# Performance work log

Measured on AMD Instinct MI355X. Metric: run time of the kernel, lower is better.

## Reference

```python
import jax, jax.numpy as jnp
import numpy as np

B, N, E = 256, 512, 8192
F_IN, DEPTH, NHID = 128, 3, 256
CAT = F_IN + DEPTH * NHID  # 896


def setup_inputs() -> dict:
    key = jax.random.key(0)
    ks = jax.random.split(key, 20)
    def w(k, shape, fan_in):
        return jax.random.normal(k, shape, jnp.float32) / np.sqrt(fan_in)
    inp = {
        "x": jax.random.normal(ks[0], (B, N, F_IN), jnp.float32),
        "edge_index": jax.random.randint(ks[1], (2, E), 0, N, jnp.int64),
        # linears: first maps F_IN->NHID, rest NHID->NHID (stacked)
        "lin0_W": w(ks[2], (F_IN, NHID), F_IN),
        "lin0_b": jnp.zeros((NHID,), jnp.float32),
        "lin_Ws": w(ks[3], (DEPTH - 1, NHID, NHID), NHID),
        "lin_bs": jnp.zeros((DEPTH - 1, NHID), jnp.float32),
        # GCNConv weights (stacked), PyG semantics: A_norm (X W) + b
        "conv_Ws": w(ks[4], (DEPTH, NHID, NHID), NHID),
        "conv_bs": jnp.zeros((DEPTH, NHID), jnp.float32),
        "sig_W": w(ks[5], (CAT, NHID), CAT),
        "sig_b": jnp.zeros((NHID,), jnp.float32),
        "tanh_W": w(ks[6], (CAT, NHID), CAT),
        "tanh_b": jnp.zeros((NHID,), jnp.float32),
        "f1_W": w(ks[7], (NHID, NHID), NHID),
        "f1_b": jnp.zeros((NHID,), jnp.float32),
        "f2_W": w(ks[8], (NHID, 2), NHID),
        "f2_b": jnp.zeros((2,), jnp.float32),
    }
    return inp


def _gcn_norm(edge_index, n):
    # add self loops, compute symmetric normalization D^-1/2 (A+I) D^-1/2
    loop = jnp.arange(n, dtype=edge_index.dtype)
    src = jnp.concatenate([edge_index[0], loop])
    dst = jnp.concatenate([edge_index[1], loop])
    deg = jax.ops.segment_sum(jnp.ones_like(src, jnp.float32), dst, num_segments=n)
    dinv = jax.lax.rsqrt(jnp.maximum(deg, 1.0))
    norm = dinv[src] * dinv[dst]  # [E+N]
    return src, dst, norm


def _gcn(h, W, b, src, dst, norm, n):
    # h: [B, N, C]
    hW = h @ W
    msg = hW[:, src, :] * norm[None, :, None]          # [B, E+N, C]
    agg = jax.vmap(lambda m: jax.ops.segment_sum(m, dst, num_segments=n))(msg)
    return agg + b


def reference(x, edge_index, lin0_W, lin0_b, lin_Ws, lin_bs, conv_Ws, conv_bs,
              sig_W, sig_b, tanh_W, tanh_b, f1_W, f1_b, f2_W, f2_b):
    n = x.shape[1]
    src, dst, norm = _gcn_norm(edge_index, n)
    xs = [x]
    out = x
    for i in range(DEPTH):
        if i == 0:
            out = out @ lin0_W + lin0_b
        else:
            out = out @ lin_Ws[i - 1] + lin_bs[i - 1]
        out = _gcn(out, conv_Ws[i], conv_bs[i], src, dst, norm, n)
        out = jnp.tanh(out)
        xs.append(out)
    cat = jnp.concatenate(xs, axis=-1)                 # [B, N, CAT]
    s = jax.nn.sigmoid(cat @ sig_W + sig_b)            # [B, N, NHID]
    t = jnp.tanh(cat @ tanh_W + tanh_b)                # [B, N, NHID]
    pooled = jnp.sum(s * t, axis=1)                    # [B, NHID] (sum over nodes)
    embeds = jnp.tanh(pooled)
    h = jax.nn.relu(embeds @ f1_W + f1_b)              # dropout is eval-mode identity
    preds = h @ f2_W + f2_b                            # [B, 2]
    preds = jnp.concatenate([jax.nn.sigmoid(preds[:, :1]), preds[:, 1:]], axis=-1)
    return preds, embeds
```

## Files before the change

### kernel.cpp

```cpp
#include <hip/hip_runtime.h>
#include <hip/hip_bf16.h>
#include <cstdint>

typedef _Float16 half_t;
typedef __attribute__((ext_vector_type(8))) _Float16 half8;
typedef __attribute__((ext_vector_type(4))) _Float16 half4;
typedef __attribute__((ext_vector_type(4))) float f32x4;

#define MFMA16x32(a, b, c) __builtin_amdgcn_mfma_f32_16x16x32_f16(a, b, c, 0, 0, 0)

static constexpr int NB  = 256;
static constexpr int NN  = 512;
static constexpr int NE  = 8192;
static constexpr int FIN = 128;
static constexpr int NH  = 256;
static constexpr int CAT = 896;

__device__ __forceinline__ void gload16(const half_t* __restrict__ g, half_t* l)
{
    __builtin_amdgcn_global_load_lds(
        (const __attribute__((address_space(1))) uint32_t*)(uintptr_t)g,
        (__attribute__((address_space(3))) uint32_t*)(uintptr_t)l, 16, 0, 0);
}

__device__ __forceinline__ void stage128x64(
    const half_t* __restrict__ src, long row0, int ldk, int k0,
    half_t* lds, int tid)
{
    const int wid = tid >> 6, lane = tid & 63;
#pragma unroll
    for (int it = 0; it < 4; ++it) {
        const int rb   = wid * 32 + it * 8;
        const int row  = rb + (lane >> 3);
        const int slot = (lane & 7) ^ (row & 7);
        gload16(src + (row0 + row) * (long)ldk + k0 + slot * 8,
                lds + (size_t)rb * 64);
    }
}

__device__ __forceinline__ half8 fragr(const half_t* lds, int row, int slot)
{
    return *(const half8*)(lds + row * 64 + ((slot ^ (row & 7)) * 8));
}

struct Tab {
    const void* src[16];
    float*      dst[16];
    int         n[16];
    int         fi[16];
    int         nseg;
};

__global__ void k_detect_all(Tab t, int* __restrict__ flags)
{
    const int s = blockIdx.x;
    if (s >= t.nseg) return;
    __shared__ int cnt_s;
    if (threadIdx.x == 0) cnt_s = 0;
    __syncthreads();
    const uint32_t* w = (const uint32_t*)t.src[s];
    int nw = t.n[s] / 2; if (nw > 2048) nw = 2048; if (nw < 1) nw = 1;
    int c = 0;
    for (int i = threadIdx.x; i < nw; i += 256) {
        const uint32_t lo = w[i] & 0xFFFFu;
        const int e = (int)((lo >> 7) & 0xFF);
        if (lo == 0u || (e >= 116 && e <= 136)) ++c;
    }
    atomicAdd(&cnt_s, c);
    __syncthreads();
    if (threadIdx.x == 0) flags[t.fi[s]] = (2 * cnt_s >= nw) ? 1 : 0;
}

__global__ void k_cvt_all(Tab t, const int* __restrict__ flags)
{
    for (int s = 0; s < t.nseg; ++s) {
        float* dst = t.dst[s];
        if (dst == nullptr) continue;
        const int is_bf = flags[t.fi[s]];
        const int n = t.n[s];
        const void* src = t.src[s];
        for (int i = blockIdx.x * 256 + threadIdx.x; i < n; i += gridDim.x * 256)
            dst[i] = is_bf
                ? __uint_as_float(((uint32_t)((const uint16_t*)src)[i]) << 16)
                : ((const float*)src)[i];
    }
}

__global__ void k_x2h(const void* __restrict__ xraw, size_t elem_off,
                      half_t* __restrict__ o, size_t n8, const int* __restrict__ flag)
{
    const int is_bf = *flag;
    const size_t gid0 = (size_t)blockIdx.x * blockDim.x + threadIdx.x;
    const size_t stride = (size_t)gridDim.x * blockDim.x;
    if (is_bf) {
        const uint4* src = (const uint4*)((const uint16_t*)xraw + elem_off);
        for (size_t i = gid0; i < n8; i += stride) {
            const uint4 v = src[i];
            half8 h;
            h[0] = (_Float16)__uint_as_float((v.x & 0xFFFFu) << 16);
            h[1] = (_Float16)__uint_as_float(v.x & 0xFFFF0000u);
            h[2] = (_Float16)__uint_as_float((v.y & 0xFFFFu) << 16);
            h[3] = (_Float16)__uint_as_float(v.y & 0xFFFF0000u);
            h[4] = (_Float16)__uint_as_float((v.z & 0xFFFFu) << 16);
            h[5] = (_Float16)__uint_as_float(v.z & 0xFFFF0000u);
            h[6] = (_Float16)__uint_as_float((v.w & 0xFFFFu) << 16);
            h[7] = (_Float16)__uint_as_float(v.w & 0xFFFF0000u);
            ((half8*)o)[i] = h;
        }
    } else {
        const float4* src = (const float4*)((const float*)xraw + elem_off);
        for (size_t i = gid0; i < n8; i += stride) {
            const float4 a = src[2 * i], b = src[2 * i + 1];
            half8 h;
            h[0] = (_Float16)a.x; h[1] = (_Float16)a.y;
            h[2] = (_Float16)a.z; h[3] = (_Float16)a.w;
            h[4] = (_Float16)b.x; h[5] = (_Float16)b.y;
            h[6] = (_Float16)b.z; h[7] = (_Float16)b.w;
            ((half8*)o)[i] = h;
        }
    }
}

__global__ void k_world(const int* __restrict__ fl, int* __restrict__ w4)
{
    if (threadIdx.x == 0) {
        const int any = fl[0] | fl[1] | fl[2] | fl[3] | fl[4] | fl[5] | fl[6];
        *w4 = any ? 0 : 1;
    }
}

__global__ void k_sentinel(__hip_bfloat16* __restrict__ out, float code)
{
    const int i = blockIdx.x * 256 + threadIdx.x;
    if (i < 66048) out[i] = __float2bfloat16(i < 512 ? code : 0.f);
}

__global__ void k_pick512(const float* __restrict__ a, const float* __restrict__ b,
                          float* __restrict__ f2Wc, float* __restrict__ linbsc)
{
    __shared__ float sa_s, sb_s;
    const int t = threadIdx.x;
    if (t == 0) { sa_s = 0.f; sb_s = 0.f; }
    __syncthreads();
    float va = fabsf(a[t]) + fabsf(a[t + 256]);
    float vb = fabsf(b[t]) + fabsf(b[t + 256]);
    for (int o = 32; o; o >>= 1) {
        va += __shfl_down(va, o, 64);
        vb += __shfl_down(vb, o, 64);
    }
    if ((t & 63) == 0) { atomicAdd(&sa_s, va); atomicAdd(&sb_s, vb); }
    __syncthreads();
    const float* f2 = (sa_s >= sb_s) ? a : b;
    const float* lb = (sa_s >= sb_s) ? b : a;
    f2Wc[t] = f2[t]; f2Wc[t + 256] = f2[t + 256];
    linbsc[t] = lb[t]; linbsc[t + 256] = lb[t + 256];
}

__global__ void k_build_graph(const int* __restrict__ ei, int* __restrict__ rowptr,
                              int* __restrict__ colx, float* __restrict__ wn,
                              float* __restrict__ srow)
{
    __shared__ int   degs[NN];
    __shared__ float dinv[NN];
    __shared__ int   rp[NN + 1];
    __shared__ int   cur[NN];
    __shared__ float sacc[NN];
    __shared__ int   is64_s;
    const int t = threadIdx.x;
    degs[t] = 0; cur[t] = 0; sacc[t] = 0.f;
    if (t == 0) {
        int orv = 0;
        for (int i = 1; i < 256; i += 2) orv |= ei[i];
        is64_s = (orv == 0) ? 1 : 0;
    }
    __syncthreads();
    const bool is64 = (is64_s != 0);
    auto EV = [&](int idx) { return is64 ? ei[2 * idx] : ei[idx]; };

    for (int e = t; e < NE; e += NN)
        atomicAdd(&degs[EV(NE + e)], 1);
    __syncthreads();
    const float dv = rsqrtf(fmaxf((float)(degs[t] + 1), 1.f));
    dinv[t] = dv;
    __syncthreads();
    if (t == 0) {
        rp[0] = 0;
        for (int i = 0; i < NN; ++i) rp[i + 1] = rp[i] + degs[i] + 1;
    }
    __syncthreads();
    rowptr[t] = rp[t];
    if (t == 0) rowptr[NN] = rp[NN];
    for (int e = t; e < NE; e += NN) {
        const int s = EV(e), d = EV(NE + e);
        const int pos = atomicAdd(&cur[d], 1);
        colx[rp[d] + pos] = s;
        wn[rp[d] + pos]   = dinv[s] * dinv[d];
        atomicAdd(&sacc[d], dinv[s]);
    }
    __syncthreads();
    const int slot = rp[t + 1] - 1;
    colx[slot] = t;
    wn[slot]   = dv * dv;
    srow[t]    = dv * (sacc[t] + dv);
}

__global__ void k_densify(const int* __restrict__ rowptr, const int* __restrict__ colx,
                          const float* __restrict__ wn, half_t* __restrict__ S16)
{
    __shared__ float row[NN];
    const int d = blockIdx.x;
    for (int i = threadIdx.x; i < NN; i += 256) row[i] = 0.f;
    __syncthreads();
    const int s0 = rowptr[d], s1 = rowptr[d + 1];
    for (int e = s0 + threadIdx.x; e < s1; e += 256)
        atomicAdd(&row[colx[e]], wn[e]);
    __syncthreads();
    for (int i = threadIdx.x; i < NN; i += 256)
        S16[(size_t)d * NN + i] = (half_t)row[i];
}

__global__ void k_fold_wc(const float* __restrict__ lin0_W, const float* __restrict__ lin_Ws,
                          const float* __restrict__ conv_Ws,
                          half_t* __restrict__ wc0, half_t* __restrict__ wc1,
                          half_t* __restrict__ wc2)
{
    const int layer = blockIdx.y;
    const int k = blockIdx.x;
    const int n = threadIdx.x;
    const int K = (layer == 0) ? FIN : NH;
    if (k >= K) return;
    const float* lin = (layer == 0) ? lin0_W : lin_Ws + (size_t)(layer - 1) * NH * NH;
    const float* cw  = conv_Ws + (size_t)layer * NH * NH;
    float s = 0.f;
    for (int j = 0; j < NH; ++j) s += lin[k * NH + j] * cw[j * NH + n];
    half_t* o = (layer == 0) ? wc0 : ((layer == 1) ? wc1 : wc2);
    o[n * K + k] = (half_t)s;
}

__global__ void k_fold_vb(const float* __restrict__ lin0_b, const float* __restrict__ lin_bs,
                          const float* __restrict__ conv_Ws, float* __restrict__ vb)
{
    const int layer = blockIdx.x, n = threadIdx.x;
    const float* lb = (layer == 0) ? lin0_b : lin_bs + (size_t)(layer - 1) * NH;
    const float* cw = conv_Ws + (size_t)layer * NH * NH;
    float s = 0.f;
    for (int j = 0; j < NH; ++j) s += lb[j] * cw[j * NH + n];
    vb[layer * NH + n] = s;
}

__global__ void k_fold_wt(const float* __restrict__ sigW, const float* __restrict__ tanW,
                          half_t* __restrict__ sh, half_t* __restrict__ th)
{
    const int n = blockIdx.x;
    const int which = blockIdx.y;
    const float* W = which ? tanW : sigW;
    half_t* o = which ? th : sh;
    for (int k = threadIdx.x; k < CAT; k += 256)
        o[(size_t)n * CAT + k] = (half_t)W[(size_t)k * NH + n];
}

__global__ __launch_bounds__(256, 2) void k_gemm_t(
    const half_t* __restrict__ A, const half_t* __restrict__ BT,
    half_t* __restrict__ hwT, int K)
{
    __shared__ __align__(16) half_t sm[17408];
    half_t* lA = sm;
    half_t* lB = sm + 8192;
    const int tid = threadIdx.x;
    const int lane = tid & 63, wid = tid >> 6;
    const int wr = wid >> 1, wc = wid & 1;
    const int row_l = lane & 15, kg = lane >> 4;
    const long mbase = (long)blockIdx.x * 128;
    const int nbase = blockIdx.y * 128;
    f32x4 acc[4][4] = {};
    for (int k0 = 0; k0 < K; k0 += 64) {
        stage128x64(A,  mbase, K, k0, lA, tid);
        stage128x64(BT, nbase, K, k0, lB, tid);
        __syncthreads();
#pragma unroll
        for (int ks = 0; ks < 2; ++ks) {
            half8 af[4], bf[4];
#pragma unroll
            for (int mt = 0; mt < 4; ++mt)
                af[mt] = fragr(lA, wr * 64 + mt * 16 + row_l, ks * 4 + kg);
#pragma unroll
            for (int nt = 0; nt < 4; ++nt)
                bf[nt] = fragr(lB, wc * 64 + nt * 16 + row_l, ks * 4 + kg);
#pragma unroll
            for (int mt = 0; mt < 4; ++mt)
#pragma unroll
                for (int nt = 0; nt < 4; ++nt)
                    acc[mt][nt] = MFMA16x32(af[mt], bf[nt], acc[mt][nt]);
        }
        __syncthreads();
    }
    half_t* lC = sm;
#pragma unroll
    for (int mt = 0; mt < 4; ++mt) {
        const int m_l = wr * 64 + mt * 16 + kg * 4;
#pragma unroll
        for (int nt = 0; nt < 4; ++nt) {
            const int n_l = wc * 64 + nt * 16 + row_l;
            half4 p;
            p[0] = (_Float16)acc[mt][nt][0]; p[1] = (_Float16)acc[mt][nt][1];
            p[2] = (_Float16)acc[mt][nt][2]; p[3] = (_Float16)acc[mt][nt][3];
            *(half4*)(lC + n_l * 136 + m_l) = p;
        }
    }
    __syncthreads();
    const int b  = (int)(mbase >> 9);
    const int s0 = (int)(mbase & 511);
#pragma unroll
    for (int pass = 0; pass < 8; ++pass) {
        const int n_l = pass * 16 + (tid >> 4);
        const int part = tid & 15;
        const half8 v = *(const half8*)(lC + n_l * 136 + part * 8);
        *(half8*)(hwT + ((size_t)b * 256 + nbase + n_l) * 512 + s0 + part * 8) = v;
    }
}

__global__ __launch_bounds__(256, 2) void k_gemm_agg(
    const half_t* __restrict__ S16, const half_t* __restrict__ hwT,
    const float* __restrict__ srow, const float* __restrict__ vb,
    const float* __restrict__ cb, half_t* __restrict__ hout)
{
    __shared__ __align__(16) half_t sm[17408];
    half_t* lA = sm;
    half_t* lB = sm + 8192;
    const int tid = threadIdx.x;
    const int lane = tid & 63, wid = tid >> 6;
    const int wr = wid >> 1, wc = wid & 1;
    const int row_l = lane & 15, kg = lane >> 4;
    const int mbase = blockIdx.x * 128;
    const int nbase = blockIdx.y * 128;
    f32x4 acc[4][4] = {};
    for (int k0 = 0; k0 < 512; k0 += 64) {
        stage128x64(S16, mbase, 512, k0, lA, tid);
        stage128x64(hwT, nbase, 512, k0, lB, tid);
        __syncthreads();
#pragma unroll
        for (int ks = 0; ks < 2; ++ks) {
            half8 af[4], bf[4];
#pragma unroll
            for (int mt = 0; mt < 4; ++mt)
                af[mt] = fragr(lA, wr * 64 + mt * 16 + row_l, ks * 4 + kg);
#pragma unroll
            for (int nt = 0; nt < 4; ++nt)
                bf[nt] = fragr(lB, wc * 64 + nt * 16 + row_l, ks * 4 + kg);
#pragma unroll
            for (int mt = 0; mt < 4; ++mt)
#pragma unroll
                for (int nt = 0; nt < 4; ++nt)
                    acc[mt][nt] = MFMA16x32(af[mt], bf[nt], acc[mt][nt]);
        }
        __syncthreads();
    }
    const int b  = nbase >> 8;
    const int c0 = nbase & 255;
    half_t* lC = sm;
#pragma unroll
    for (int mt = 0; mt < 4; ++mt) {
        const int m_l = wr * 64 + mt * 16 + kg * 4;
        float sr[4];
#pragma unroll
        for (int r = 0; r < 4; ++r) sr[r] = srow[mbase + m_l + r];
#pragma unroll
        for (int nt = 0; nt < 4; ++nt) {
            const int n_l = wc * 64 + nt * 16 + row_l;
            const float vbc = vb[c0 + n_l], cbc = cb[c0 + n_l];
#pragma unroll
            for (int r = 0; r < 4; ++r)
                lC[(m_l + r) * 136 + n_l] =
                    (half_t)tanhf(acc[mt][nt][r] + sr[r] * vbc + cbc);
        }
    }
    __syncthreads();
#pragma unroll
    for (int pass = 0; pass < 8; ++pass) {
        const int row = pass * 16 + (tid >> 4);
        const int col = (tid & 15) * 8;
        const half8 v = *(const half8*)(lC + row * 136 + col);
        *(half8*)(hout + ((size_t)b * NN + mbase + row) * NH + c0 + col) = v;
    }
}

__global__ __launch_bounds__(256, 2) void k_gemm_final(
    const half_t* __restrict__ x16, const half_t* __restrict__ h1,
    const half_t* __restrict__ h2, const half_t* __restrict__ h3,
    const half_t* __restrict__ bsh, const half_t* __restrict__ bth,
    const float* __restrict__ sig_b, const float* __restrict__ tan_b,
    float* __restrict__ part)
{
    __shared__ __align__(16) half_t sm[24576];
    __shared__ float red[2][128];
    half_t* lA  = sm;
    half_t* lBs = sm + 8192;
    half_t* lBt = sm + 16384;
    const int tid = threadIdx.x;
    const int lane = tid & 63, wid = tid >> 6;
    const int wr = wid >> 1, wc = wid & 1;
    const int row_l = lane & 15, kg = lane >> 4;
    const long mbase = (long)blockIdx.x * 128;
    const int sup = blockIdx.y;
    f32x4 aS[4][4] = {}, aT[4][4] = {};
    for (int kt = 0; kt < 14; ++kt) {
        const int k0 = kt * 64;
        const half_t* Aseg; int segK, lk;
        if (k0 < 128)      { Aseg = x16; segK = 128; lk = k0; }
        else if (k0 < 384) { Aseg = h1;  segK = 256; lk = k0 - 128; }
        else if (k0 < 640) { Aseg = h2;  segK = 256; lk = k0 - 384; }
        else               { Aseg = h3;  segK = 256; lk = k0 - 640; }
        stage128x64(Aseg, mbase, segK, lk, lA, tid);
        stage128x64(bsh, (long)sup * 128, CAT, k0, lBs, tid);
        stage128x64(bth, (long)sup * 128, CAT, k0, lBt, tid);
        __syncthreads();
#pragma unroll
        for (int ks = 0; ks < 2; ++ks) {
            half8 af[4];
#pragma unroll
            for (int mt = 0; mt < 4; ++mt)
                af[mt] = fragr(lA, wr * 64 + mt * 16 + row_l, ks * 4 + kg);
#pragma unroll
            for (int nt = 0; nt < 4; ++nt) {
                const int r = wc * 64 + nt * 16 + row_l;
                const half8 fs = fragr(lBs, r, ks * 4 + kg);
                const half8 ft = fragr(lBt, r, ks * 4 + kg);
#pragma unroll
                for (int mt = 0; mt < 4; ++mt) {
                    aS[mt][nt] = MFMA16x32(af[mt], fs, aS[mt][nt]);
                    aT[mt][nt] = MFMA16x32(af[mt], ft, aT[mt][nt]);
                }
            }
        }
        __syncthreads();
    }
#pragma unroll
    for (int nt = 0; nt < 4; ++nt) {
        const int j = sup * 128 + wc * 64 + nt * 16 + row_l;
        const float sb = sig_b[j], tb = tan_b[j];
        float ps = 0.f;
#pragma unroll
        for (int mt = 0; mt < 4; ++mt)
#pragma unroll
            for (int r = 0; r < 4; ++r) {
                const float u = aS[mt][nt][r] + sb;
                const float v = aT[mt][nt][r] + tb;
                ps += (1.f / (1.f + expf(-u))) * tanhf(v);
            }
        ps += __shfl_xor(ps, 16, 64);
        ps += __shfl_xor(ps, 32, 64);
        if (lane < 16) red[wr][wc * 64 + nt * 16 + lane] = ps;
    }
    __syncthreads();
    if (tid < 128)
        part[(long)blockIdx.x * 256 + sup * 128 + tid] = red[0][tid] + red[1][tid];
}

__global__ __launch_bounds__(256) void k_finish(
    const float* __restrict__ part, const float* __restrict__ f1W,
    const float* __restrict__ f1b, const float* __restrict__ f2W,
    const float* __restrict__ f2b, void* __restrict__ dout,
    const int* __restrict__ w4)
{
    __shared__ float e[NH], h[NH];
    const int b = blockIdx.x, t = threadIdx.x;
    const float* p = part + (size_t)b * 1024 + t;
    const float ev = tanhf(p[0] + p[256] + p[512] + p[768]);
    e[t] = ev;
    if (*w4) ((float*)dout)[512 + b * NH + t] = ev;
    else     ((__hip_bfloat16*)dout)[512 + b * NH + t] = __float2bfloat16(ev);
    __syncthreads();
    float a = f1b[t];
    for (int k = 0; k < NH; ++k) a += e[k] * f1W[k * NH + t];
    h[t] = fmaxf(a, 0.f);
    __syncthreads();
    if (t < 64) {
        float p0 = 0.f, p1 = 0.f;
        for (int jj = t; jj < NH; jj += 64) {
            p0 += h[jj] * f2W[jj * 2 + 0];
            p1 += h[jj] * f2W[jj * 2 + 1];
        }
        for (int o = 32; o; o >>= 1) {
            p0 += __shfl_down(p0, o, 64);
            p1 += __shfl_down(p1, o, 64);
        }
        if (t == 0) {
            p0 += f2b[0]; p1 += f2b[1];
            p0 = 1.f / (1.f + expf(-p0));
            if (*w4) {
                ((float*)dout)[b * 2 + 0] = p0;
                ((float*)dout)[b * 2 + 1] = p1;
            } else {
                ((__hip_bfloat16*)dout)[b * 2 + 0] = __float2bfloat16(p0);
                ((__hip_bfloat16*)dout)[b * 2 + 1] = __float2bfloat16(p1);
            }
        }
    }
}

extern "C" void kernel_launch(void* const* d_in, const int* in_sizes, int n_in,
                              void* d_out, int out_size, void* d_ws, size_t ws_size,
                              hipStream_t stream)
{
    (void)out_size;

    int ix = -1, ie = -1, il0 = -1, ilw = -1, icw = -1, icb = -1, if1 = -1, if2b = -1;
    int i229[2] = {-1, -1}; int n229 = 0;
    int i512[2] = {-1, -1}; int n512 = 0;
    int i256[4] = {-1, -1, -1, -1}; int n256 = 0;
    int bad = 0;
    for (int i = 0; i < n_in && i < 16; ++i) {
        switch (in_sizes[i]) {
            case 16777216: ix = i; break;
            case 16384:    ie = i; break;
            case 32768:    il0 = i; break;
            case 131072:   ilw = i; break;
            case 196608:   icw = i; break;
            case 768:      icb = i; break;
            case 65536:    if1 = i; break;
            case 2:        if2b = i; break;
            case 229376:   if (n229 < 2) i229[n229++] = i; else bad = 1; break;
            case 512:      if (n512 < 2) i512[n512++] = i; else bad = 1; break;
            case 256:      if (n256 < 4) i256[n256++] = i; else bad = 1; break;
            default:       bad = 1; break;
        }
    }
    if (n_in != 16 || bad || ix < 0 || ie < 0 || il0 < 0 || ilw < 0 || icw < 0 ||
        icb < 0 || if1 < 0 || if2b < 0 || n229 != 2 || n512 != 2 || n256 != 4) {
        k_sentinel<<<(66048 + 255) / 256, 256, 0, stream>>>((__hip_bfloat16*)d_out, 20480.f);
        return;
    }

    char* wp = (char*)d_ws;
    auto alloc = [&](size_t sz) {
        char* p = wp;
        wp += (sz + 4095) & ~(size_t)4095;
        return p;
    };
    int*   flags  = (int*)alloc(32 * 4);
    int*   w4     = (int*)alloc(64);
    float* c_lin0W  = (float*)alloc((size_t)FIN * NH * 4);
    float* c_linWs  = (float*)alloc((size_t)2 * NH * NH * 4);
    float* c_convWs = (float*)alloc((size_t)3 * NH * NH * 4);
    float* c_convbs = (float*)alloc((size_t)3 * NH * 4);
    float* c_sigW   = (float*)alloc((size_t)CAT * NH * 4);
    float* c_tanW   = (float*)alloc((size_t)CAT * NH * 4);
    float* c_f1W    = (float*)alloc((size_t)NH * NH * 4);
    float* c_f2b    = (float*)alloc(2 * 4);
    float* c_512a   = (float*)alloc(512 * 4);
    float* c_512b   = (float*)alloc(512 * 4);
    float* f2Wc     = (float*)alloc(512 * 4);
    float* linbsc   = (float*)alloc(512 * 4);
    float* c_b256[4];
    for (int q = 0; q < 4; ++q) c_b256[q] = (float*)alloc(256 * 4);
    int*    rowptr = (int*)alloc((NN + 1) * 4);
    int*    colx   = (int*)alloc((NE + NN) * 4);
    float*  wn     = (float*)alloc((NE + NN) * 4);
    float*  srow   = (float*)alloc(NN * 4);
    float*  vb     = (float*)alloc(3 * NH * 4);
    half_t* S16  = (half_t*)alloc((size_t)NN * NN * 2);
    half_t* wc0  = (half_t*)alloc((size_t)NH * FIN * 2);
    half_t* wc1  = (half_t*)alloc((size_t)NH * NH * 2);
    half_t* wc2  = (half_t*)alloc((size_t)NH * NH * 2);
    half_t* sgh  = (half_t*)alloc((size_t)NH * CAT * 2);
    half_t* tnh  = (half_t*)alloc((size_t)NH * CAT * 2);
    float*  part = (float*)alloc((size_t)1024 * 256 * 4);
    float*  emb  = (float*)alloc((size_t)NB * NH * 4);

    const size_t fixed_end = (size_t)(wp - (char*)d_ws);
    int CB = 256;
    while (CB > 4) {
        const size_t mc = (size_t)CB * NN;
        const size_t act = ((mc * FIN * 2 + 4095) & ~(size_t)4095) +
                           4 * ((mc * NH * 2 + 4095) & ~(size_t)4095);
        if (fixed_end + act + (1u << 20) <= ws_size) break;
        CB >>= 1;
    }
    const size_t MC = (size_t)CB * NN;
    const int NCH = NB / CB;

    half_t* x16c = (half_t*)alloc(MC * FIN * 2);
    half_t* h1c  = (half_t*)alloc(MC * NH * 2);
    half_t* h2c  = (half_t*)alloc(MC * NH * 2);
    half_t* h3c  = (half_t*)alloc(MC * NH * 2);
    half_t* hwT  = (half_t*)alloc(MC * NH * 2);

    Tab t = {};
    int s = 0;
    auto addseg = [&](int idx, float* dst, int n, int fi) {
        t.src[s] = d_in[idx]; t.dst[s] = dst; t.n[s] = n; t.fi[s] = fi; ++s;
    };
    addseg(ix,      nullptr,   16777216, 0);
    addseg(il0,     c_lin0W,   FIN * NH, 1);
    addseg(ilw,     c_linWs,   2 * NH * NH, 2);
    addseg(icw,     c_convWs,  3 * NH * NH, 3);
    addseg(i229[0], c_sigW,    CAT * NH, 4);
    addseg(i229[1], c_tanW,    CAT * NH, 5);
    addseg(if1,     c_f1W,     NH * NH, 6);
    addseg(i512[0], c_512a,    512, 7);
    addseg(i512[1], c_512b,    512, 8);
    for (int q = 0; q < 4; ++q) addseg(i256[q], c_b256[q], 256, 9 + q);
    addseg(icb,     c_convbs,  3 * NH, 13);
    addseg(if2b,    c_f2b,     2, 14);
    t.nseg = s;

    k_detect_all<<<t.nseg, 256, 0, stream>>>(t, flags);
    k_world<<<1, 64, 0, stream>>>(flags, w4);
    k_cvt_all<<<1024, 256, 0, stream>>>(t, flags);
    k_pick512<<<1, 256, 0, stream>>>(c_512a, c_512b, f2Wc, linbsc);

    const float* lin0_b = c_b256[0];
    const float* sig_b  = c_b256[1];
    const float* tan_b  = c_b256[2];
    const float* f1_b   = c_b256[3];
    (void)emb;

    k_build_graph<<<1, 512, 0, stream>>>((const int*)d_in[ie], rowptr, colx, wn, srow);
    k_densify<<<NN, 256, 0, stream>>>(rowptr, colx, wn, S16);
    k_fold_wc<<<dim3(256, 3), 256, 0, stream>>>(c_lin0W, c_linWs, c_convWs, wc0, wc1, wc2);
    k_fold_vb<<<3, 256, 0, stream>>>(lin0_b, linbsc, c_convWs, vb);
    k_fold_wt<<<dim3(256, 2), 256, 0, stream>>>(c_sigW, c_tanW, sgh, tnh);

    for (int c = 0; c < NCH; ++c) {
        k_x2h<<<2048, 256, 0, stream>>>(d_in[ix], (size_t)c * MC * FIN, x16c,
                                        MC * FIN / 8, flags + 0);
        k_gemm_t<<<dim3(CB * 4, 2), 256, 0, stream>>>(x16c, wc0, hwT, 128);
        k_gemm_agg<<<dim3(4, CB * 2), 256, 0, stream>>>(S16, hwT, srow, vb + 0,
                                                        c_convbs + 0, h1c);
        k_gemm_t<<<dim3(CB * 4, 2), 256, 0, stream>>>(h1c, wc1, hwT, 256);
        k_gemm_agg<<<dim3(4, CB * 2), 256, 0, stream>>>(S16, hwT, srow, vb + 256,
                                                        c_convbs + 256, h2c);
        k_gemm_t<<<dim3(CB * 4, 2), 256, 0, stream>>>(h2c, wc2, hwT, 256);
        k_gemm_agg<<<dim3(4, CB * 2), 256, 0, stream>>>(S16, hwT, srow, vb + 512,
                                                        c_convbs + 512, h3c);
        k_gemm_final<<<dim3(CB * 4, 2), 256, 0, stream>>>(
            x16c, h1c, h2c, h3c, sgh, tnh, sig_b, tan_b,
            part + (size_t)c * CB * 1024);
    }
    k_finish<<<NB, 256, 0, stream>>>(part, c_f1W, f1_b, f2Wc, c_f2b, d_out, w4);
}
```

Baseline: 542.1 us.

## Swizzle GEMM blocks across XCDs, merge small kernels, convert x once

Adds an XCD-aware workgroup remap to the three GEMM kernels so that neighbouring tiles land on the same chiplet and can share L2. Removes the k_world and k_fold_vb launches by folding their work into k_finish and k_fold_wt. Converts the whole x input to fp16 in one launch instead of once per chunk. This cuts launch overhead and may improve cache locality, but it needs a full-size fp16 x buffer, which changes the workspace chunk sizing, and the swizzle assumes the workgroup count divides evenly by 8.

Measured after the change: 514.5 us. -5.1%, faster.

```diff
diff --git a/kernel.cpp b/kernel.cpp
--- a/kernel.cpp
+++ b/kernel.cpp
@@ -15,6 +15,15 @@
 static constexpr int FIN = 128;
 static constexpr int NH  = 256;
 static constexpr int CAT = 896;
+
+__device__ __forceinline__ void xcd_swz(int& bx, int& by)
+{
+    const int nwg = gridDim.x * gridDim.y;
+    int wgid = blockIdx.y * gridDim.x + blockIdx.x;
+    wgid = (wgid & 7) * (nwg >> 3) + (wgid >> 3);
+    bx = wgid % gridDim.x;
+    by = wgid / gridDim.x;
+}
 
 __device__ __forceinline__ void gload16(const half_t* __restrict__ g, half_t* l)
 {
@@ -86,14 +95,14 @@
     }
 }
 
-__global__ void k_x2h(const void* __restrict__ xraw, size_t elem_off,
-                      half_t* __restrict__ o, size_t n8, const int* __restrict__ flag)
+__global__ void k_x2h(const void* __restrict__ xraw, half_t* __restrict__ o,
+                      size_t n8, const int* __restrict__ flag)
 {
     const int is_bf = *flag;
     const size_t gid0 = (size_t)blockIdx.x * blockDim.x + threadIdx.x;
     const size_t stride = (size_t)gridDim.x * blockDim.x;
     if (is_bf) {
-        const uint4* src = (const uint4*)((const uint16_t*)xraw + elem_off);
+        const uint4* src = (const uint4*)xraw;
         for (size_t i = gid0; i < n8; i += stride) {
             const uint4 v = src[i];
             half8 h;
@@ -108,7 +117,7 @@
             ((half8*)o)[i] = h;
         }
     } else {
-        const float4* src = (const float4*)((const float*)xraw + elem_off);
+        const float4* src = (const float4*)xraw;
         for (size_t i = gid0; i < n8; i += stride) {
             const float4 a = src[2 * i], b = src[2 * i + 1];
             half8 h;
@@ -118,14 +127,6 @@
             h[6] = (_Float16)b.z; h[7] = (_Float16)b.w;
             ((half8*)o)[i] = h;
         }
-    }
-}
-
-__global__ void k_world(const int* __restrict__ fl, int* __restrict__ w4)
-{
-    if (threadIdx.x == 0) {
-        const int any = fl[0] | fl[1] | fl[2] | fl[3] | fl[4] | fl[5] | fl[6];
-        *w4 = any ? 0 : 1;
     }
 }
 
@@ -237,22 +238,24 @@
     o[n * K + k] = (half_t)s;
 }
 
-__global__ void k_fold_vb(const float* __restrict__ lin0_b, const float* __restrict__ lin_bs,
+__global__ void k_fold_wt(const float* __restrict__ sigW, const float* __restrict__ tanW,
+                          half_t* __restrict__ sh, half_t* __restrict__ th,
+                          const float* __restrict__ lin0_b, const float* __restrict__ lin_bs,
                           const float* __restrict__ conv_Ws, float* __restrict__ vb)
 {
-    const int layer = blockIdx.x, n = threadIdx.x;
-    const float* lb = (layer == 0) ? lin0_b : lin_bs + (size_t)(layer - 1) * NH;
-    const float* cw = conv_Ws + (size_t)layer * NH * NH;
-    float s = 0.f;
-    for (int j = 0; j < NH; ++j) s += lb[j] * cw[j * NH + n];
-    vb[layer * NH + n] = s;
-}
-
-__global__ void k_fold_wt(const float* __restrict__ sigW, const float* __restrict__ tanW,
-                          half_t* __restrict__ sh, half_t* __restrict__ th)
-{
+    const int which = blockIdx.y;
+    if (which == 2) {
+        const int layer = blockIdx.x;
+        if (layer >= 3) return;
+        const int n = threadIdx.x;
+        const float* lb = (layer == 0) ? lin0_b : lin_bs + (size_t)(layer - 1) * NH;
+        const float* cw = conv_Ws + (size_t)layer * NH * NH;
+        float s = 0.f;
+        for (int j = 0; j < NH; ++j) s += lb[j] * cw[j * NH + n];
+        vb[layer * NH + n] = s;
+        return;
+    }
     const int n = blockIdx.x;
-    const int which = blockIdx.y;
     const float* W = which ? tanW : sigW;
     half_t* o = which ? th : sh;
     for (int k = threadIdx.x; k < CAT; k += 256)
@@ -266,12 +269,13 @@
     __shared__ __align__(16) half_t sm[17408];
     half_t* lA = sm;
     half_t* lB = sm + 8192;
+    int bx, by; xcd_swz(bx, by);
     const int tid = threadIdx.x;
     const int lane = tid & 63, wid = tid >> 6;
     const int wr = wid >> 1, wc = wid & 1;
     const int row_l = lane & 15, kg = lane >> 4;
-    const long mbase = (long)blockIdx.x * 128;
-    const int nbase = blockIdx.y * 128;
+    const long mbase = (long)bx * 128;
+    const int nbase = by * 128;
     f32x4 acc[4][4] = {};
     for (int k0 = 0; k0 < K; k0 += 64) {
         stage128x64(A,  mbase, K, k0, lA, tid);
@@ -327,12 +331,13 @@
     __shared__ __align__(16) half_t sm[17408];
     half_t* lA = sm;
     half_t* lB = sm + 8192;
+    int bx, by; xcd_swz(bx, by);
     const int tid = threadIdx.x;
     const int lane = tid & 63, wid = tid >> 6;
     const int wr = wid >> 1, wc = wid & 1;
     const int row_l = lane & 15, kg = lane >> 4;
-    const int mbase = blockIdx.x * 128;
-    const int nbase = blockIdx.y * 128;
+    const int mbase = bx * 128;
+    const int nbase = by * 128;
     f32x4 acc[4][4] = {};
     for (int k0 = 0; k0 < 512; k0 += 64) {
         stage128x64(S16, mbase, 512, k0, lA, tid);
@@ -396,12 +401,13 @@
     half_t* lA  = sm;
     half_t* lBs = sm + 8192;
     half_t* lBt = sm + 16384;
+    int bx, by; xcd_swz(bx, by);
     const int tid = threadIdx.x;
     const int lane = tid & 63, wid = tid >> 6;
     const int wr = wid >> 1, wc = wid & 1;
     const int row_l = lane & 15, kg = lane >> 4;
-    const long mbase = (long)blockIdx.x * 128;
-    const int sup = blockIdx.y;
+    const long mbase = (long)bx * 128;
+    const int sup = by;
     f32x4 aS[4][4] = {}, aT[4][4] = {};
     for (int kt = 0; kt < 14; ++kt) {
         const int k0 = kt * 64;
@@ -453,22 +459,25 @@
     }
     __syncthreads();
     if (tid < 128)
-        part[(long)blockIdx.x * 256 + sup * 128 + tid] = red[0][tid] + red[1][tid];
+        part[(long)bx * 256 + sup * 128 + tid] = red[0][tid] + red[1][tid];
 }
 
 __global__ __launch_bounds__(256) void k_finish(
     const float* __restrict__ part, const float* __restrict__ f1W,
     const float* __restrict__ f1b, const float* __restrict__ f2W,
     const float* __restrict__ f2b, void* __restrict__ dout,
-    const int* __restrict__ w4)
+    const int* __restrict__ flags)
 {
     __shared__ float e[NH], h[NH];
     const int b = blockIdx.x, t = threadIdx.x;
+    const int any = flags[0] | flags[1] | flags[2] | flags[3] | flags[4] |
+                    flags[5] | flags[6];
+    const int w4 = any ? 0 : 1;
     const float* p = part + (size_t)b * 1024 + t;
     const float ev = tanhf(p[0] + p[256] + p[512] + p[768]);
     e[t] = ev;
-    if (*w4) ((float*)dout)[512 + b * NH + t] = ev;
-    else     ((__hip_bfloat16*)dout)[512 + b * NH + t] = __float2bfloat16(ev);
+    if (w4) ((float*)dout)[512 + b * NH + t] = ev;
+    else    ((__hip_bfloat16*)dout)[512 + b * NH + t] = __float2bfloat16(ev);
     __syncthreads();
     float a = f1b[t];
     for (int k = 0; k < NH; ++k) a += e[k] * f1W[k * NH + t];
@@ -487,7 +496,7 @@
         if (t == 0) {
             p0 += f2b[0]; p1 += f2b[1];
             p0 = 1.f / (1.f + expf(-p0));
-            if (*w4) {
+            if (w4) {
                 ((float*)dout)[b * 2 + 0] = p0;
                 ((float*)dout)[b * 2 + 1] = p1;
             } else {
@@ -538,7 +547,6 @@
         return p;
     };
     int*   flags  = (int*)alloc(32 * 4);
-    int*   w4     = (int*)alloc(64);
     float* c_lin0W  = (float*)alloc((size_t)FIN * NH * 4);
     float* c_linWs  = (float*)alloc((size_t)2 * NH * NH * 4);
     float* c_convWs = (float*)alloc((size_t)3 * NH * NH * 4);
@@ -565,21 +573,19 @@
     half_t* sgh  = (half_t*)alloc((size_t)NH * CAT * 2);
     half_t* tnh  = (half_t*)alloc((size_t)NH * CAT * 2);
     float*  part = (float*)alloc((size_t)1024 * 256 * 4);
-    float*  emb  = (float*)alloc((size_t)NB * NH * 4);
+    half_t* x16  = (half_t*)alloc((size_t)NB * NN * FIN * 2);
 
     const size_t fixed_end = (size_t)(wp - (char*)d_ws);
     int CB = 256;
     while (CB > 4) {
         const size_t mc = (size_t)CB * NN;
-        const size_t act = ((mc * FIN * 2 + 4095) & ~(size_t)4095) +
-                           4 * ((mc * NH * 2 + 4095) & ~(size_t)4095);
+        const size_t act = 4 * ((mc * NH * 2 + 4095) & ~(size_t)4095);
         if (fixed_end + act + (1u << 20) <= ws_size) break;
         CB >>= 1;
     }
     const size_t MC = (size_t)CB * NN;
     const int NCH = NB / CB;
 
-    half_t* x16c = (half_t*)alloc(MC * FIN * 2);
     half_t* h1c  = (half_t*)alloc(MC * NH * 2);
     half_t* h2c  = (half_t*)alloc(MC * NH * 2);
     half_t* h3c  = (half_t*)alloc(MC * NH * 2);
@@ -605,7 +611,6 @@
     t.nseg = s;
 
     k_detect_all<<<t.nseg, 256, 0, stream>>>(t, flags);
-    k_world<<<1, 64, 0, stream>>>(flags, w4);
     k_cvt_all<<<1024, 256, 0, stream>>>(t, flags);
     k_pick512<<<1, 256, 0, stream>>>(c_512a, c_512b, f2Wc, linbsc);
 
@@ -613,17 +618,16 @@
     const float* sig_b  = c_b256[1];
     const float* tan_b  = c_b256[2];
     const float* f1_b   = c_b256[3];
-    (void)emb;
 
     k_build_graph<<<1, 512, 0, stream>>>((const int*)d_in[ie], rowptr, colx, wn, srow);
     k_densify<<<NN, 256, 0, stream>>>(rowptr, colx, wn, S16);
     k_fold_wc<<<dim3(256, 3), 256, 0, stream>>>(c_lin0W, c_linWs, c_convWs, wc0, wc1, wc2);
-    k_fold_vb<<<3, 256, 0, stream>>>(lin0_b, linbsc, c_convWs, vb);
-    k_fold_wt<<<dim3(256, 2), 256, 0, stream>>>(c_sigW, c_tanW, sgh, tnh);
+    k_fold_wt<<<dim3(256, 3), 256, 0, stream>>>(c_sigW, c_tanW, sgh, tnh,
+                                                lin0_b, linbsc, c_convWs, vb);
+    k_x2h<<<2048, 256, 0, stream>>>(d_in[ix], x16, (size_t)NB * NN * FIN / 8, flags + 0);
 
     for (int c = 0; c < NCH; ++c) {
-        k_x2h<<<2048, 256, 0, stream>>>(d_in[ix], (size_t)c * MC * FIN, x16c,
-                                        MC * FIN / 8, flags + 0);
+        half_t* x16c = x16 + (size_t)c * MC * FIN;
         k_gemm_t<<<dim3(CB * 4, 2), 256, 0, stream>>>(x16c, wc0, hwT, 128);
         k_gemm_agg<<<dim3(4, CB * 2), 256, 0, stream>>>(S16, hwT, srow, vb + 0,
                                                         c_convbs + 0, h1c);
@@ -637,5 +641,5 @@
             x16c, h1c, h2c, h3c, sgh, tnh, sig_b, tan_b,
             part + (size_t)c * CB * 1024);
     }
-    k_finish<<<NB, 256, 0, stream>>>(part, c_f1W, f1_b, f2Wc, c_f2b, d_out, w4);
-}
+    k_finish<<<NB, 256, 0, stream>>>(part, c_f1W, f1_b, f2Wc, c_f2b, d_out, flags);
+}
```
